# Performance work log

Hardware: AMD Instinct MI355X
Metric: run time of the kernel (lower is better)

The kernel has to match this reference:

```python
import jax, jax.numpy as jnp
import numpy as np

B, L, C = 4, 3072, 21
P = 96        # input_token_len
OUT = 96      # output_token_len
D = 1024      # d_model
H = 16        # n_heads
NL = 2        # e_layers
DFF = 4096    # d_ff


def setup_inputs() -> dict:
    key = jax.random.key(0)
    ks = iter(jax.random.split(key, 64))
    def nrm(shape, s=0.02):
        return jax.random.normal(next(ks), shape, dtype=jnp.float32) * s
    z = lambda shape: jnp.zeros(shape, jnp.float32)
    o = lambda shape: jnp.ones(shape, jnp.float32)
    return {
        "x": jax.random.normal(next(ks), (B, L, C), dtype=jnp.float32),
        "x_mark": z((B, L, 4)),
        "y_mark": z((B, L, 4)),
        # windowed embedding Linear(P -> D)
        "emb_W": nrm((P, D)), "emb_b": z((D,)),
        # per-layer attention projections (stacked over layers)
        "Wq": nrm((NL, D, D)), "bq": z((NL, D)),
        "Wk": nrm((NL, D, D)), "bk": z((NL, D)),
        "Wv": nrm((NL, D, D)), "bv": z((NL, D)),
        "Wo": nrm((NL, D, D)), "bo": z((NL, D)),
        # per-layer FFN
        "W1": nrm((NL, D, DFF)), "b1": z((NL, DFF)),
        "W2": nrm((NL, DFF, D)), "b2": z((NL, D)),
        # per-layer LayerNorms + final norm
        "ln1_s": o((NL, D)), "ln1_b": z((NL, D)),
        "ln2_s": o((NL, D)), "ln2_b": z((NL, D)),
        "lnf_s": o((D,)), "lnf_b": z((D,)),
        "head_W": nrm((D, OUT)), "head_b": z((OUT,)),
        # MLP classifier OUT -> 256 -> 64 -> 2
        "c1_W": nrm((OUT, 256), 0.1), "c1_b": z((256,)),
        "c2_W": nrm((256, 64), 0.1), "c2_b": z((64,)),
        "c3_W": nrm((64, 2), 0.1), "c3_b": z((2,)),
    }


def _layer_norm(zx, s, b, eps=1e-5):
    m = zx.mean(-1, keepdims=True)
    v = ((zx - m) ** 2).mean(-1, keepdims=True)
    return (zx - m) / jnp.sqrt(v + eps) * s + b


def reference(x, x_mark, y_mark, emb_W, emb_b, Wq, bq, Wk, bk, Wv, bv, Wo, bo,
              W1, b1, W2, b2, ln1_s, ln1_b, ln2_s, ln2_b, lnf_s, lnf_b,
              head_W, head_b, c1_W, c1_b, c2_W, c2_b, c3_W, c3_b):
    # --- instance normalization over time (means detached, as in torch) ---
    means = jax.lax.stop_gradient(x.mean(1, keepdims=True))
    xc = x - means
    stdev = jnp.maximum(jnp.sqrt(xc.var(axis=1, keepdims=True) + 1e-6), 1e-5)
    xn = xc / stdev
    Bb, Ll, Cc = xn.shape
    Nn = Ll // P
    # unfold: [B, C, N, P] (step == size, non-overlapping windows)
    xt = xn.transpose(0, 2, 1).reshape(Bb, Cc, Nn, P)
    h = (xt @ emb_W + emb_b).reshape(Bb, Cc * Nn, D)  # [B, C*N, D], variable-major
    # Timer multivariate mask: kron(ones(C,C), tril(N,N)) -> allowed positions
    tok = jnp.arange(Nn)
    causal = tok[None, :] <= tok[:, None]              # [N, N]
    allowed = jnp.tile(causal, (Cc, Cc))               # [C*N, C*N]
    scale = 1.0 / np.sqrt(D // H)
    for l in range(Wq.shape[0]):
        q = (h @ Wq[l] + bq[l]).reshape(Bb, -1, H, D // H)
        k = (h @ Wk[l] + bk[l]).reshape(Bb, -1, H, D // H)
        v = (h @ Wv[l] + bv[l]).reshape(Bb, -1, H, D // H)
        scores = jnp.einsum("blhe,bshe->bhls", q, k)
        scores = jnp.where(allowed[None, None], scores * scale, -jnp.inf)
        A = jax.nn.softmax(scores, axis=-1)
        att = jnp.einsum("bhls,bshe->blhe", A, v).reshape(Bb, -1, D)
        att = att @ Wo[l] + bo[l]
        h = _layer_norm(h + att, ln1_s[l], ln1_b[l])
        y = jax.nn.gelu(h @ W1[l] + b1[l], approximate=False) @ W2[l] + b2[l]
        h = _layer_norm(h + y, ln2_s[l], ln2_b[l])
    h = _layer_norm(h, lnf_s, lnf_b)
    # head + double mean pooling over variables and tokens
    dec = (h @ head_W + head_b).reshape(Bb, Cc, Nn, OUT)
    feat = dec.mean(axis=(1, 2))                       # [B, OUT]
    feat = jnp.nan_to_num(feat, nan=0.0, posinf=0.0, neginf=0.0)
    z1 = jax.nn.relu(feat @ c1_W + c1_b)
    z2 = jax.nn.relu(z1 @ c2_W + c2_b)
    logits = z2 @ c3_W + c3_b                          # [B, n_classes]
    return logits
```

## Files before the change

kernel.cpp:

```cpp
#include <hip/hip_runtime.h>
#include <hip/hip_bf16.h>
#include <math.h>


typedef unsigned short u16;
typedef __attribute__((ext_vector_type(8))) __bf16 bf16x8;
typedef __attribute__((ext_vector_type(4))) float f32x4;

#define DEVI __device__ __forceinline__

DEVI u16 f2b(float f){
  union { float f; unsigned u; } x; x.f = f;
  unsigned r = x.u + 0x7fffu + ((x.u >> 16) & 1u);
  return (u16)(r >> 16);
}

DEVI void gload16(const void* g, void* l){
  __builtin_amdgcn_global_load_lds(
      (const __attribute__((address_space(1))) unsigned int*)g,
      (__attribute__((address_space(3))) unsigned int*)l,
      16, 0, 0);
}

DEVI float block_sum(float v){
  __shared__ float lds[4];
  #pragma unroll
  for (int o = 32; o > 0; o >>= 1) v += __shfl_xor(v, o);
  if ((threadIdx.x & 63) == 0) lds[threadIdx.x >> 6] = v;
  __syncthreads();
  v = lds[0] + lds[1] + lds[2] + lds[3];
  __syncthreads();
  return v;
}

DEVI float block_max(float v){
  __shared__ float lds[4];
  #pragma unroll
  for (int o = 32; o > 0; o >>= 1) v = fmaxf(v, __shfl_xor(v, o));
  if ((threadIdx.x & 63) == 0) lds[threadIdx.x >> 6] = v;
  __syncthreads();
  v = fmaxf(fmaxf(lds[0], lds[1]), fmaxf(lds[2], lds[3]));
  __syncthreads();
  return v;
}

template<int BM, int BN, int EPI>
__global__ __launch_bounds__(256) void gemm2(
    const u16* __restrict__ A0, long sA1, long sA2, int lda,
    const u16* __restrict__ B0, long sB1, long sB2, int ldb,
    float* __restrict__ Cf0, long sCf1, long sCf2, int ldc,
    u16* __restrict__ Cb0, long sCb1, long sCb2, int ldcb,
    const float* __restrict__ bias,
    int M, int N, int K, int Kchunk, int zdiv, int sw)
{
  constexpr int WM = BM/2, WN = BN/2, FM = WM/16, FN = WN/16;
  constexpr int RA = (BM*4)/256, RB = (BN*4)/256;

  const int nbn = gridDim.x, nbm = gridDim.y;
  const int per = nbm * nbn;
  const int nwg = per * gridDim.z;
  int gid = ((int)blockIdx.z * nbm + (int)blockIdx.y) * nbn + (int)blockIdx.x;
  int q = nwg >> 3, r = nwg & 7, xcd = gid & 7, pos = gid >> 3;
  int cid = (xcd < r ? xcd*(q+1) : r*(q+1) + (xcd-r)*q) + pos;
  int z = cid / per, rem = cid % per;
  int bm, bn;
  {
    int stripe = rem / (sw*nbm), loc = rem % (sw*nbm);
    bm = loc / sw; bn = stripe*sw + loc % sw;
  }

  const int zq = z / zdiv, zr = z % zdiv;
  const long k0 = (long)zr * Kchunk;
  const u16* A = A0 + zq*sA1 + zr*sA2 + k0;
  const u16* B = B0 + zq*sB1 + zr*sB2 + k0;

  const int tid = threadIdx.x;
  const int lane = tid & 63, wave = tid >> 6;
  const int l16 = lane & 15, lk = lane >> 4;
  const int wr = wave >> 1, wc = wave & 1;
  const int m0 = bm * BM, n0 = bn * BN;

  __shared__ u16 sA[2][4*BM*8];
  __shared__ u16 sB[2][4*BN*8];

  const u16* abase[RA];
  #pragma unroll
  for (int it = 0; it < RA; ++it){
    int s = it*256 + tid;
    int row = s >> 2, kgS = s & 3;
    int col8 = kgS ^ (row & 3);
    int gr = m0 + row; if (gr > M-1) gr = M-1;
    abase[it] = A + (long)gr*lda + col8*8;
  }
  const u16* bbase[RB];
  #pragma unroll
  for (int it = 0; it < RB; ++it){
    int s = it*256 + tid;
    int row = s >> 2, kgS = s & 3;
    int col8 = kgS ^ (row & 3);
    int gc = n0 + row; if (gc > N-1) gc = N-1;
    bbase[it] = B + (long)gc*ldb + col8*8;
  }

  auto stage = [&](int buf, int kt){
    #pragma unroll
    for (int it = 0; it < RA; ++it)
      gload16(abase[it] + kt, &sA[buf][(it*256 + tid)*8]);
    #pragma unroll
    for (int it = 0; it < RB; ++it)
      gload16(bbase[it] + kt, &sB[buf][(it*256 + tid)*8]);
  };

  f32x4 acc[FM][FN];
  const f32x4 z4 = {0.f, 0.f, 0.f, 0.f};
  #pragma unroll
  for (int i = 0; i < FM; ++i)
    #pragma unroll
    for (int j = 0; j < FN; ++j) acc[i][j] = z4;

  const int nk = K >> 5;
  stage(0, 0);
  __syncthreads();
  int cur = 0;
  for (int t = 0; t < nk; ++t){
    if (t + 1 < nk) stage(cur ^ 1, (t + 1) << 5);
    bf16x8 af[FM], bf[FN];
    #pragma unroll
    for (int fm = 0; fm < FM; ++fm){
      int row = wr*WM + fm*16 + l16;
      af[fm] = *(const bf16x8*)&sA[cur][(row*4 + (lk ^ (row & 3)))*8];
    }
    #pragma unroll
    for (int fn = 0; fn < FN; ++fn){
      int col = wc*WN + fn*16 + l16;
      bf[fn] = *(const bf16x8*)&sB[cur][(col*4 + (lk ^ (col & 3)))*8];
    }
    #pragma unroll
    for (int fm = 0; fm < FM; ++fm)
      #pragma unroll
      for (int fn = 0; fn < FN; ++fn)
        acc[fm][fn] = __builtin_amdgcn_mfma_f32_16x16x32_bf16(af[fm], bf[fn], acc[fm][fn], 0, 0, 0);
    __syncthreads();
    cur ^= 1;
  }

  float* Cf = (EPI==0 || EPI==1) ? Cf0 + zq*sCf1 + zr*sCf2 : nullptr;
  u16*  Cb = (EPI!=0) ? Cb0 + zq*sCb1 + zr*sCb2 : nullptr;
  #pragma unroll
  for (int fm = 0; fm < FM; ++fm){
    #pragma unroll
    for (int fn = 0; fn < FN; ++fn){
      int col = n0 + wc*WN + fn*16 + l16;
      if (col < N){
        float bv = bias ? bias[col] : 0.f;
        #pragma unroll
        for (int i = 0; i < 4; ++i){
          int row = m0 + wr*WM + fm*16 + lk*4 + i;
          if (row < M){
            float v = acc[fm][fn][i] + bv;
            if (EPI == 3) v = 0.5f * v * (1.f + erff(v * 0.70710678118f));
            if (EPI == 0 || EPI == 1) Cf[(long)row*ldc + col] = v;
            if (EPI != 0) Cb[(long)row*ldcb + col] = f2b(v);
          }
        }
      }
    }
  }
}

__global__ __launch_bounds__(256) void flash_attn(
    const u16* __restrict__ qkv, const u16* __restrict__ vt,
    u16* __restrict__ att)
{
  const int qt = blockIdx.x, bh = blockIdx.y;
  const int b = bh >> 4, h = bh & 15;
  const int tid = threadIdx.x, lane = tid & 63, w = tid >> 6;
  const int l16 = lane & 15, lk = lane >> 4;

  __shared__ u16 P_lds[4][16][72];

  const int qrow = qt*64 + w*16 + l16;
  const int qc = qrow < 672 ? qrow : 671;
  const int qn = qc & 31;

  const u16* qbase = qkv + ((long)b*672 + qc)*3072 + h*64;
  bf16x8 qf[2];
  qf[0] = *(const bf16x8*)(qbase + lk*8);
  qf[1] = *(const bf16x8*)(qbase + 32 + lk*8);

  const u16* kbase = qkv + (long)b*672*3072 + 1024 + h*64;
  const u16* vbase = vt + (long)bh*64*672;

  f32x4 oacc[4];
  const f32x4 z4 = {0.f,0.f,0.f,0.f};
  #pragma unroll
  for (int j = 0; j < 4; ++j) oacc[j] = z4;
  float m_run = -1e30f, lsum = 0.f;

  for (int t = 0; t < 11; ++t){
    const int kv0 = t*64;
    bf16x8 kf[4][2];
    #pragma unroll
    for (int j = 0; j < 4; ++j){
      int krow = kv0 + j*16 + l16; if (krow > 671) krow = 671;
      const u16* kp = kbase + (long)krow*3072 + lk*8;
      kf[j][0] = *(const bf16x8*)(kp);
      kf[j][1] = *(const bf16x8*)(kp + 32);
    }
    bf16x8 vf[4][2];
    #pragma unroll
    for (int j = 0; j < 4; ++j){
      const u16* vp = vbase + (long)(j*16 + l16)*672 + kv0 + lk*8;
      vf[j][0] = *(const bf16x8*)(vp);
      vf[j][1] = *(const bf16x8*)(vp + 32);
    }

    f32x4 sacc[4];
    __builtin_amdgcn_s_setprio(1);
    #pragma unroll
    for (int j = 0; j < 4; ++j){
      sacc[j] = z4;
      sacc[j] = __builtin_amdgcn_mfma_f32_16x16x32_bf16(kf[j][0], qf[0], sacc[j], 0, 0, 0);
      sacc[j] = __builtin_amdgcn_mfma_f32_16x16x32_bf16(kf[j][1], qf[1], sacc[j], 0, 0, 0);
    }
    __builtin_amdgcn_s_setprio(0);

    float vals[16];
    float mx = -1e30f;
    #pragma unroll
    for (int j = 0; j < 4; ++j)
      #pragma unroll
      for (int i = 0; i < 4; ++i){
        int kv = kv0 + j*16 + lk*4 + i;
        bool ok = ((kv & 31) <= qn) && (kv < 672);
        float v = ok ? sacc[j][i] * 0.125f : -1e30f;
        vals[j*4+i] = v;
        mx = fmaxf(mx, v);
      }
    mx = fmaxf(mx, __shfl_xor(mx, 16));
    mx = fmaxf(mx, __shfl_xor(mx, 32));
    float m_new = fmaxf(m_run, mx);
    float alpha = __expf(m_run - m_new);
    float ps = 0.f;
    #pragma unroll
    for (int i = 0; i < 16; ++i){
      float e = (vals[i] > -1e29f) ? __expf(vals[i] - m_new) : 0.f;
      vals[i] = e; ps += e;
    }
    ps += __shfl_xor(ps, 16);
    ps += __shfl_xor(ps, 32);
    lsum = lsum * alpha + ps;
    m_run = m_new;
    #pragma unroll
    for (int j = 0; j < 4; ++j)
      #pragma unroll
      for (int i = 0; i < 4; ++i) oacc[j][i] *= alpha;

    #pragma unroll
    for (int j = 0; j < 4; ++j){
      unsigned lo = (unsigned)f2b(vals[j*4+0]) | ((unsigned)f2b(vals[j*4+1]) << 16);
      unsigned hi = (unsigned)f2b(vals[j*4+2]) | ((unsigned)f2b(vals[j*4+3]) << 16);
      unsigned long long pk = (unsigned long long)lo | ((unsigned long long)hi << 32);
      *(unsigned long long*)&P_lds[w][l16][j*16 + lk*4] = pk;
    }

    bf16x8 pf0 = *(const bf16x8*)&P_lds[w][l16][lk*8];
    bf16x8 pf1 = *(const bf16x8*)&P_lds[w][l16][32 + lk*8];
    __builtin_amdgcn_s_setprio(1);
    #pragma unroll
    for (int j = 0; j < 4; ++j){
      oacc[j] = __builtin_amdgcn_mfma_f32_16x16x32_bf16(vf[j][0], pf0, oacc[j], 0, 0, 0);
      oacc[j] = __builtin_amdgcn_mfma_f32_16x16x32_bf16(vf[j][1], pf1, oacc[j], 0, 0, 0);
    }
    __builtin_amdgcn_s_setprio(0);
  }

  if (qrow < 672){
    float inv = 1.f / lsum;
    u16* orow = att + ((long)b*672 + qrow)*1024 + h*64;
    #pragma unroll
    for (int j = 0; j < 4; ++j){
      unsigned lo = (unsigned)f2b(oacc[j][0]*inv) | ((unsigned)f2b(oacc[j][1]*inv) << 16);
      unsigned hi = (unsigned)f2b(oacc[j][2]*inv) | ((unsigned)f2b(oacc[j][3]*inv) << 16);
      unsigned long long pk = (unsigned long long)lo | ((unsigned long long)hi << 32);
      *(unsigned long long*)(orow + j*16 + lk*4) = pk;
    }
  }
}


__global__ __launch_bounds__(256) void instnorm_stats(
    const float* __restrict__ x, float* __restrict__ mean, float* __restrict__ rstd)
{
  int bc = blockIdx.x;
  int b = bc / 21, c = bc % 21;
  const float* p = x + (long)b*3072*21 + c;
  float s = 0.f, sq = 0.f;
  for (int l = threadIdx.x; l < 3072; l += 256){
    float u = p[(long)l*21];
    s += u; sq += u*u;
  }
  s = block_sum(s); sq = block_sum(sq);
  if (threadIdx.x == 0){
    float m = s * (1.f/3072.f);
    float var = sq * (1.f/3072.f) - m*m;
    float sd = fmaxf(sqrtf(var + 1e-6f), 1e-5f);
    mean[bc] = m; rstd[bc] = 1.f / sd;
  }
}

__global__ __launch_bounds__(256) void build_windows(
    const float* __restrict__ x, const float* __restrict__ mean,
    const float* __restrict__ rstd, u16* __restrict__ xw)
{
  int idx = blockIdx.x*256 + threadIdx.x;
  if (idx >= 2688*96) return;
  int r = idx / 96, p = idx % 96;
  int b = r / 672, rem = r % 672, c = rem / 32, n = rem % 32;
  int l = n*96 + p;
  int bc = b*21 + c;
  float u = (x[((long)b*3072 + l)*21 + c] - mean[bc]) * rstd[bc];
  xw[idx] = f2b(u);
}

__global__ __launch_bounds__(256) void transpose_cast(
    const float* __restrict__ in, long sIn, u16* __restrict__ out, long sOut,
    int R, int C)
{
  in += (long)blockIdx.z * sIn; out += (long)blockIdx.z * sOut;
  __shared__ float tile[32][33];
  int ct = blockIdx.x, rt = blockIdx.y;
  int tx = threadIdx.x & 31, ty = threadIdx.x >> 5;
  #pragma unroll
  for (int i = 0; i < 4; ++i){
    int r = rt*32 + ty + i*8, c = ct*32 + tx;
    tile[ty+i*8][tx] = (r < R && c < C) ? in[(long)r*C + c] : 0.f;
  }
  __syncthreads();
  #pragma unroll
  for (int i = 0; i < 4; ++i){
    int oc = rt*32 + tx;
    int orow = ct*32 + ty + i*8;
    if (orow < C && oc < R) out[(long)orow*R + oc] = f2b(tile[tx][ty+i*8]);
  }
}

__global__ __launch_bounds__(256) void transpose_sq(
    const float* __restrict__ Wq, const float* __restrict__ Wk,
    const float* __restrict__ Wv, const float* __restrict__ Wo,
    u16* __restrict__ wqkvT, u16* __restrict__ woT)
{
  int zz = blockIdx.z, l = zz >> 2, t = zz & 3;
  const float* src = (t==0) ? Wq : (t==1) ? Wk : (t==2) ? Wv : Wo;
  src += (size_t)l*1024*1024;
  u16* dst = (t < 3) ? wqkvT + (size_t)l*3072*1024 + (size_t)t*1024*1024
                     : woT + (size_t)l*1024*1024;
  __shared__ float tile[32][33];
  int ct = blockIdx.x, rt = blockIdx.y;
  int tx = threadIdx.x & 31, ty = threadIdx.x >> 5;
  #pragma unroll
  for (int i = 0; i < 4; ++i)
    tile[ty+i*8][tx] = src[(long)(rt*32 + ty + i*8)*1024 + ct*32 + tx];
  __syncthreads();
  #pragma unroll
  for (int i = 0; i < 4; ++i)
    dst[(long)(ct*32 + ty + i*8)*1024 + rt*32 + tx] = f2b(tile[tx][ty+i*8]);
}

__global__ __launch_bounds__(256) void transpose_vt(
    const u16* __restrict__ qkv, u16* __restrict__ vt)
{
  int zz = blockIdx.z; int b = zz >> 4, hh = zz & 15;
  const u16* in = qkv + (long)b*672*3072 + 2048 + hh*64;
  u16* out = vt + (long)zz*64*672;
  __shared__ u16 tile[32][33];
  int ct = blockIdx.x, rt = blockIdx.y;
  int tx = threadIdx.x & 31, ty = threadIdx.x >> 5;
  #pragma unroll
  for (int i = 0; i < 4; ++i){
    int s = rt*32 + ty + i*8, e = ct*32 + tx;
    tile[ty+i*8][tx] = in[(long)s*3072 + e];
  }
  __syncthreads();
  #pragma unroll
  for (int i = 0; i < 4; ++i){
    int e = ct*32 + ty + i*8, s = rt*32 + tx;
    out[(long)e*672 + s] = tile[tx][ty+i*8];
  }
}

__global__ __launch_bounds__(256) void concat_qkv_bias(
    const float* __restrict__ bq, const float* __restrict__ bk,
    const float* __restrict__ bv, float* __restrict__ bqkv)
{
  int i = blockIdx.x*256 + threadIdx.x;
  if (i >= 2*3072) return;
  int l = i / 3072, j = i % 3072;
  float v = (j < 1024) ? bq[l*1024 + j]
          : (j < 2048) ? bk[l*1024 + j - 1024]
                       : bv[l*1024 + j - 2048];
  bqkv[i] = v;
}

__global__ __launch_bounds__(256) void ln_kernel(
    const float* __restrict__ X, const float* __restrict__ R, int nsl, long ssl,
    const float* __restrict__ cb,
    const float* __restrict__ g, const float* __restrict__ be,
    float* __restrict__ outF, u16* __restrict__ outB)
{
  long row = blockIdx.x;
  long base = row * 1024;
  int d4 = threadIdx.x * 4;
  float4 v = *(const float4*)&X[base + d4];
  for (int sl = 0; sl < nsl; ++sl){
    float4 rv = *(const float4*)&R[(long)sl*ssl + base + d4];
    v.x += rv.x; v.y += rv.y; v.z += rv.z; v.w += rv.w;
  }
  if (cb){
    float4 cv = *(const float4*)&cb[d4];
    v.x += cv.x; v.y += cv.y; v.z += cv.z; v.w += cv.w;
  }
  float s = v.x + v.y + v.z + v.w;
  float sq = v.x*v.x + v.y*v.y + v.z*v.z + v.w*v.w;
  s = block_sum(s); sq = block_sum(sq);
  float mean = s * (1.f/1024.f);
  float var = sq * (1.f/1024.f) - mean*mean;
  float rst = rsqrtf(var + 1e-5f);
  float4 gv = *(const float4*)&g[d4];
  float4 bv = *(const float4*)&be[d4];
  float o0 = (v.x - mean) * rst * gv.x + bv.x;
  float o1 = (v.y - mean) * rst * gv.y + bv.y;
  float o2 = (v.z - mean) * rst * gv.z + bv.z;
  float o3 = (v.w - mean) * rst * gv.w + bv.w;
  if (outF){
    float4 ov = {o0, o1, o2, o3};
    *(float4*)&outF[base + d4] = ov;
  }
  if (outB){
    unsigned lo = (unsigned)f2b(o0) | ((unsigned)f2b(o1) << 16);
    unsigned hi = (unsigned)f2b(o2) | ((unsigned)f2b(o3) << 16);
    unsigned long long pk = (unsigned long long)lo | ((unsigned long long)hi << 32);
    *(unsigned long long*)&outB[base + d4] = pk;
  }
}

__global__ __launch_bounds__(256) void pool_kernel(
    const float* __restrict__ dec, const float* __restrict__ headB,
    float* __restrict__ feat)
{
  int b = blockIdx.x, o = blockIdx.y;
  float s = 0.f;
  for (int i = threadIdx.x; i < 672*8; i += 256){
    int sl = i / 672, r = i % 672;
    s += dec[(long)sl*2688*96 + ((long)b*672 + r)*96 + o];
  }
  s = block_sum(s);
  if (threadIdx.x == 0){
    float f = headB[o] + s * (1.f/672.f);
    if (!isfinite(f)) f = 0.f;
    feat[b*96 + o] = f;
  }
}

__global__ __launch_bounds__(256) void classifier(
    const float* __restrict__ feat,
    const float* __restrict__ w1, const float* __restrict__ b1,
    const float* __restrict__ w2, const float* __restrict__ b2,
    const float* __restrict__ w3, const float* __restrict__ b3,
    float* __restrict__ out)
{
  __shared__ float f[384];
  __shared__ float z1[1024];
  __shared__ float z2[256];
  int t = threadIdx.x;
  for (int i = t; i < 384; i += 256) f[i] = feat[i];
  __syncthreads();
  for (int o = t; o < 1024; o += 256){
    int b = o >> 8, j = o & 255;
    float s = b1[j];
    for (int p = 0; p < 96; ++p) s += f[b*96 + p] * w1[p*256 + j];
    z1[o] = fmaxf(s, 0.f);
  }
  __syncthreads();
  for (int o = t; o < 256; o += 256){
    int b = o >> 6, j = o & 63;
    float s = b2[j];
    for (int p = 0; p < 256; ++p) s += z1[b*256 + p] * w2[p*64 + j];
    z2[o] = fmaxf(s, 0.f);
  }
  __syncthreads();
  if (t < 8){
    int b = t >> 1, j = t & 1;
    float s = b3[j];
    for (int p = 0; p < 64; ++p) s += z2[b*64 + p] * w3[p*2 + j];
    out[t] = s;
  }
}


static inline int pick_sw(int nbn){
  if (nbn % 8 == 0) return 8;
  if (nbn % 4 == 0) return 4;
  if (nbn % 2 == 0) return 2;
  return 1;
}

extern "C" void kernel_launch(void* const* d_in, const int* in_sizes, int n_in,
                              void* d_out, int out_size, void* d_ws, size_t ws_size,
                              hipStream_t stream)
{
  (void)in_sizes; (void)n_in; (void)out_size; (void)ws_size;
  const float* x     = (const float*)d_in[0];
  const float* embW  = (const float*)d_in[3];
  const float* embB  = (const float*)d_in[4];
  const float* Wq    = (const float*)d_in[5];
  const float* bq    = (const float*)d_in[6];
  const float* Wk    = (const float*)d_in[7];
  const float* bk    = (const float*)d_in[8];
  const float* Wv    = (const float*)d_in[9];
  const float* bv    = (const float*)d_in[10];
  const float* Wo    = (const float*)d_in[11];
  const float* bo    = (const float*)d_in[12];
  const float* W1    = (const float*)d_in[13];
  const float* b1    = (const float*)d_in[14];
  const float* W2    = (const float*)d_in[15];
  const float* b2    = (const float*)d_in[16];
  const float* ln1s  = (const float*)d_in[17];
  const float* ln1b  = (const float*)d_in[18];
  const float* ln2s  = (const float*)d_in[19];
  const float* ln2b  = (const float*)d_in[20];
  const float* lnfs  = (const float*)d_in[21];
  const float* lnfb  = (const float*)d_in[22];
  const float* headW = (const float*)d_in[23];
  const float* headB = (const float*)d_in[24];
  const float* c1W   = (const float*)d_in[25];
  const float* c1B   = (const float*)d_in[26];
  const float* c2W   = (const float*)d_in[27];
  const float* c2B   = (const float*)d_in[28];
  const float* c3W   = (const float*)d_in[29];
  const float* c3B   = (const float*)d_in[30];
  float* out = (float*)d_out;

  char* w = (char*)d_ws; size_t off = 0;
  auto alloc = [&](size_t bytes)->void*{
    void* p = w + off; off = (off + bytes + 255) & ~(size_t)255; return p; };
  u16*   embT  = (u16*)alloc((size_t)96*1024*2);
  u16*   wqkvT = (u16*)alloc((size_t)2*3072*1024*2);
  u16*   woT   = (u16*)alloc((size_t)2*1024*1024*2);
  u16*   w1T   = (u16*)alloc((size_t)2*4096*1024*2);
  u16*   w2T   = (u16*)alloc((size_t)2*1024*4096*2);
  u16*   headT = (u16*)alloc((size_t)96*1024*2);
  float* bqkv  = (float*)alloc((size_t)2*3072*4);
  float* meanp = (float*)alloc(84*4);
  float* rstdp = (float*)alloc(84*4);
  u16*   xw    = (u16*)alloc((size_t)2688*96*2);
  float* h     = (float*)alloc((size_t)2688*1024*4);
  u16*   hb    = (u16*)alloc((size_t)2688*1024*2);
  u16*   qkv   = (u16*)alloc((size_t)2688*3072*2);
  u16*   vt    = (u16*)alloc((size_t)64*64*672*2);
  u16*   att   = (u16*)alloc((size_t)2688*1024*2);
  float* feat  = (float*)alloc(384*4);
  size_t un_off = off;
  float* tmp  = (float*)(w + un_off);
  u16*   ffnb = (u16*)(w + un_off + (size_t)2*2688*1024*4);
  float* dec  = (float*)(w + un_off);

  transpose_sq<<<dim3(32,32,8), 256, 0, stream>>>(Wq, Wk, Wv, Wo, wqkvT, woT);
  transpose_cast<<<dim3(32,3,1),  256, 0, stream>>>(embW, 0, embT, 0, 96, 1024);
  transpose_cast<<<dim3(3,32,1),  256, 0, stream>>>(headW, 0, headT, 0, 1024, 96);
  transpose_cast<<<dim3(128,32,2),256, 0, stream>>>(W1, (long)1024*4096, w1T, (long)4096*1024, 1024, 4096);
  transpose_cast<<<dim3(32,128,2),256, 0, stream>>>(W2, (long)4096*1024, w2T, (long)1024*4096, 4096, 1024);
  concat_qkv_bias<<<(2*3072+255)/256, 256, 0, stream>>>(bq, bk, bv, bqkv);

  instnorm_stats<<<84, 256, 0, stream>>>(x, meanp, rstdp);
  build_windows<<<(2688*96+255)/256, 256, 0, stream>>>(x, meanp, rstdp, xw);

  gemm2<128,128,1><<<dim3(8,21,1),256,0,stream>>>(
      xw,0,0,96, embT,0,0,96, h,0,0,1024, hb,0,0,1024, embB,
      2688,1024,96,0,1, pick_sw(8));

  for (int l = 0; l < 2; ++l){
    gemm2<128,128,2><<<dim3(24,21,1),256,0,stream>>>(
        hb,0,0,1024, wqkvT+(size_t)l*3072*1024,0,0,1024,
        nullptr,0,0,0, qkv,0,0,3072, bqkv+l*3072,
        2688,3072,1024,0,1, pick_sw(24));
    transpose_vt<<<dim3(2,21,64),256,0,stream>>>(qkv, vt);

    flash_attn<<<dim3(11,64),256,0,stream>>>(qkv, vt, att);

    gemm2<128,128,0><<<dim3(8,21,2),256,0,stream>>>(
        att,0,0,1024, woT+(size_t)l*1024*1024,0,0,1024,
        tmp,0,(long)2688*1024,1024, nullptr,0,0,0, nullptr,
        2688,1024,512,512,2, pick_sw(8));
    ln_kernel<<<2688,256,0,stream>>>(h, tmp, 2, (long)2688*1024, bo+l*1024,
                                     ln1s+l*1024, ln1b+l*1024, h, hb);
    gemm2<128,128,3><<<dim3(32,21,1),256,0,stream>>>(
        hb,0,0,1024, w1T+(size_t)l*4096*1024,0,0,1024,
        nullptr,0,0,0, ffnb,0,0,4096, b1+l*4096,
        2688,4096,1024,0,1, pick_sw(32));
    gemm2<128,128,0><<<dim3(8,21,2),256,0,stream>>>(
        ffnb,0,0,4096, w2T+(size_t)l*4096*1024,0,0,4096,
        tmp,0,(long)2688*1024,1024, nullptr,0,0,0, nullptr,
        2688,1024,2048,2048,2, pick_sw(8));
    ln_kernel<<<2688,256,0,stream>>>(h, tmp, 2, (long)2688*1024, b2+l*1024,
                                     ln2s+l*1024, ln2b+l*1024, h, hb);
  }

  ln_kernel<<<2688,256,0,stream>>>(h, nullptr, 0, 0, nullptr, lnfs, lnfb, nullptr, hb);
  gemm2<128,128,0><<<dim3(1,21,8),256,0,stream>>>(
      hb,0,0,1024, headT,0,0,1024,
      dec,0,(long)2688*96,96, nullptr,0,0,0, nullptr,
      2688,96,128,128,8, pick_sw(1));
  pool_kernel<<<dim3(4,96),256,0,stream>>>(dec, headB, feat);
  classifier<<<1,256,0,stream>>>(feat, c1W,c1B, c2W,c2B, c3W,c3B, out);
}
```

Measured before the change: 564.3 us.

## Triple-buffer GEMM LDS staging with explicit waitcnt and one barrier per step

Moves the bf16 GEMM main loop from a double-buffered LDS scheme with two __syncthreads per k-step to a three-slot ring. Tiles are prefetched two steps ahead, and partial vmcnt waits plus a single s_barrier per iteration keep one tile in flight during compute. It also changes the LDS XOR swizzle to key on row>>1, aiming to reduce bank conflicts in the MFMA fragment reads. The cost is 50% more shared memory per block, which may lower occupancy, and the hand-written waitcnt logic depends on the exact number of outstanding loads. The diff also deletes the unused block_max helper.

```diff
diff --git a/kernel.cpp b/kernel.cpp
--- a/kernel.cpp
+++ b/kernel.cpp
@@ -29,17 +29,6 @@
   if ((threadIdx.x & 63) == 0) lds[threadIdx.x >> 6] = v;
   __syncthreads();
   v = lds[0] + lds[1] + lds[2] + lds[3];
-  __syncthreads();
-  return v;
-}
-
-DEVI float block_max(float v){
-  __shared__ float lds[4];
-  #pragma unroll
-  for (int o = 32; o > 0; o >>= 1) v = fmaxf(v, __shfl_xor(v, o));
-  if ((threadIdx.x & 63) == 0) lds[threadIdx.x >> 6] = v;
-  __syncthreads();
-  v = fmaxf(fmaxf(lds[0], lds[1]), fmaxf(lds[2], lds[3]));
   __syncthreads();
   return v;
 }
@@ -55,6 +44,7 @@
 {
   constexpr int WM = BM/2, WN = BN/2, FM = WM/16, FN = WN/16;
   constexpr int RA = (BM*4)/256, RB = (BN*4)/256;
+  constexpr int VM = RA + RB;
 
   const int nbn = gridDim.x, nbm = gridDim.y;
   const int per = nbm * nbn;
@@ -80,15 +70,15 @@
   const int wr = wave >> 1, wc = wave & 1;
   const int m0 = bm * BM, n0 = bn * BN;
 
-  __shared__ u16 sA[2][4*BM*8];
-  __shared__ u16 sB[2][4*BN*8];
+  __shared__ u16 sA[3][4*BM*8];
+  __shared__ u16 sB[3][4*BN*8];
 
   const u16* abase[RA];
   #pragma unroll
   for (int it = 0; it < RA; ++it){
     int s = it*256 + tid;
     int row = s >> 2, kgS = s & 3;
-    int col8 = kgS ^ (row & 3);
+    int col8 = kgS ^ ((row >> 1) & 3);
     int gr = m0 + row; if (gr > M-1) gr = M-1;
     abase[it] = A + (long)gr*lda + col8*8;
   }
@@ -97,7 +87,7 @@
   for (int it = 0; it < RB; ++it){
     int s = it*256 + tid;
     int row = s >> 2, kgS = s & 3;
-    int col8 = kgS ^ (row & 3);
+    int col8 = kgS ^ ((row >> 1) & 3);
     int gc = n0 + row; if (gc > N-1) gc = N-1;
     bbase[it] = B + (long)gc*ldb + col8*8;
   }
@@ -120,28 +110,35 @@
 
   const int nk = K >> 5;
   stage(0, 0);
-  __syncthreads();
-  int cur = 0;
+  if (nk > 1) stage(1, 32);
   for (int t = 0; t < nk; ++t){
-    if (t + 1 < nk) stage(cur ^ 1, (t + 1) << 5);
+    asm volatile("s_waitcnt lgkmcnt(0)" ::: "memory");
+    if (t + 1 < nk) asm volatile("s_waitcnt vmcnt(%0)" :: "i"(VM) : "memory");
+    else            asm volatile("s_waitcnt vmcnt(0)" ::: "memory");
+    __builtin_amdgcn_sched_barrier(0);
+    __builtin_amdgcn_s_barrier();
+    __builtin_amdgcn_sched_barrier(0);
+
+    const int slot = t % 3;
     bf16x8 af[FM], bf[FN];
     #pragma unroll
     for (int fm = 0; fm < FM; ++fm){
       int row = wr*WM + fm*16 + l16;
-      af[fm] = *(const bf16x8*)&sA[cur][(row*4 + (lk ^ (row & 3)))*8];
+      af[fm] = *(const bf16x8*)&sA[slot][(row*4 + (lk ^ ((row >> 1) & 3)))*8];
     }
     #pragma unroll
     for (int fn = 0; fn < FN; ++fn){
       int col = wc*WN + fn*16 + l16;
-      bf[fn] = *(const bf16x8*)&sB[cur][(col*4 + (lk ^ (col & 3)))*8];
+      bf[fn] = *(const bf16x8*)&sB[slot][(col*4 + (lk ^ ((col >> 1) & 3)))*8];
     }
     #pragma unroll
     for (int fm = 0; fm < FM; ++fm)
       #pragma unroll
       for (int fn = 0; fn < FN; ++fn)
         acc[fm][fn] = __builtin_amdgcn_mfma_f32_16x16x32_bf16(af[fm], bf[fn], acc[fm][fn], 0, 0, 0);
-    __syncthreads();
-    cur ^= 1;
+
+    if (t + 2 < nk) stage((t + 2) % 3, (t + 2) << 5);
+    __builtin_amdgcn_sched_barrier(0);
   }
 
   float* Cf = (EPI==0 || EPI==1) ? Cf0 + zq*sCf1 + zr*sCf2 : nullptr;
```

Result: faster. 536.0 us, median of 3 (-5.0%).
